# Kernel optimization log

Measured on AMD Instinct MI355X. Metric: run time of the kernel, lower is better.

Reference implementation:

```python
import jax, jax.numpy as jnp
import numpy as np

D = 1024        # model dim (== moe_inter_dim, required by Expert's x2*x3)
H = 1024        # expert hidden dim (moe_inter_dim)
E = 8           # n_routed_experts
K = 2           # n_activated_experts (top-k)
I = 2 * 1024    # shared-expert inter dim = n_shared_experts * moe_inter_dim
ROUTE_SCALE = 1.0


def setup_inputs() -> dict:
    key = jax.random.key(0)
    ks = jax.random.split(key, 12)
    s = lambda *sh: 1.0 / np.sqrt(sh[-1])
    return {
        "x":      jax.random.normal(ks[0], (1, 2048, D), jnp.float32),
        "gate_w": jax.random.normal(ks[1], (E, D), jnp.float32) * s(E, D),
        "w1":     jax.random.normal(ks[2], (E, H, D), jnp.float32) * s(H, D),
        "b1":     jax.random.normal(ks[3], (E, H), jnp.float32) * 0.01,
        "w2":     jax.random.normal(ks[4], (E, D, H), jnp.float32) * s(D, H),
        "b2":     jax.random.normal(ks[5], (E, D), jnp.float32) * 0.01,
        "w3":     jax.random.normal(ks[6], (E, H, D), jnp.float32) * s(H, D),
        "b3":     jax.random.normal(ks[7], (E, H), jnp.float32) * 0.01,
        "sw1":    jax.random.normal(ks[8], (I, D), jnp.float32) * s(I, D),
        "sw2":    jax.random.normal(ks[9], (I, D), jnp.float32) * s(I, D),
        "sw3":    jax.random.normal(ks[10], (D, I), jnp.float32) * s(D, I),
    }


def reference(x, gate_w, w1, b1, w2, b2, w3, b3, sw1, sw2, sw3):
    B, S, _ = x.shape
    xt = x.reshape(-1, D)                                  # (T, D)
    # ---- Gate (softmax scoring, n_groups==1, no bias, route_scale=1) ----
    logits = xt @ gate_w.T                                 # (T, E)
    scores = jax.nn.softmax(logits.astype(jnp.float32), axis=-1)
    top_vals, idx = jax.lax.top_k(scores, K)               # (T, K)
    weights = (jnp.take_along_axis(scores, idx, axis=1)
               .astype(x.dtype)) * ROUTE_SCALE             # (T, K)
    # ---- Routed experts: input is scaled by routing weight BEFORE expert ----
    xs = xt[:, None, :] * weights[:, :, None]              # (T, K, D)
    y = jnp.zeros_like(xt)
    for e in range(E):  # fixed small loop over experts (dense masked dispatch)
        mask = (idx == e).astype(x.dtype)                  # (T, K)
        h = jax.nn.silu(jnp.einsum('tkd,hd->tkh', xs, w1[e]) + b1[e])
        x2 = jnp.einsum('tkh,dh->tkd', h, w2[e]) + b2[e]   # (T, K, D)
        x3 = jnp.einsum('tkd,hd->tkh', xs, w3[e]) + b3[e]  # (T, K, H==D)
        y = y + jnp.sum((x2 * x3) * mask[:, :, None], axis=1)
    # ---- Shared experts (SwiGLU MLP, no biases) ----
    z = (jax.nn.silu(xt @ sw1.T) * (xt @ sw2.T)) @ sw3.T   # (T, D)
    return (y + z).reshape(B, S, D)
```

## Files before the change

kernel.cpp:

```cpp
#include <hip/hip_runtime.h>

typedef unsigned short u16;
typedef __attribute__((ext_vector_type(4))) float floatx4;
typedef __attribute__((ext_vector_type(8))) short short8;

#define MAXROWS 5120
#define MAXMT 40

__device__ __forceinline__ u16 f2bf(float f) {
    union { float f; unsigned u; } v; v.f = f;
    unsigned r = v.u + 0x7FFF + ((v.u >> 16) & 1);
    return (u16)(r >> 16);
}
__device__ __forceinline__ float bf2f(u16 h) {
    union { unsigned u; float f; } v; v.u = ((unsigned)h) << 16; return v.f;
}
__device__ __forceinline__ float silu_f(float x) { return x / (1.f + __expf(-x)); }

__device__ __forceinline__ void gl_lds16(const void* g, void* l) {
    __builtin_amdgcn_global_load_lds(
        (__attribute__((address_space(1))) unsigned int*)g,
        (__attribute__((address_space(3))) unsigned int*)l, 16, 0, 0);
}

__device__ __forceinline__ void ld_frags(
    unsigned a0, unsigned a1, unsigned a2, unsigned a3,
    unsigned b0, unsigned b1, unsigned b2, unsigned b3,
    short8& af0, short8& af1, short8& af2, short8& af3,
    short8& bf0, short8& bf1, short8& bf2, short8& bf3) {
    asm volatile(
        "ds_read_b128 %0, %8\n\t"
        "ds_read_b128 %1, %9\n\t"
        "ds_read_b128 %2, %10\n\t"
        "ds_read_b128 %3, %11\n\t"
        "ds_read_b128 %4, %12\n\t"
        "ds_read_b128 %5, %13\n\t"
        "ds_read_b128 %6, %14\n\t"
        "ds_read_b128 %7, %15\n\t"
        "s_waitcnt lgkmcnt(0)"
        : "=&v"(af0), "=&v"(af1), "=&v"(af2), "=&v"(af3),
          "=&v"(bf0), "=&v"(bf1), "=&v"(bf2), "=&v"(bf3)
        : "v"(a0), "v"(a1), "v"(a2), "v"(a3),
          "v"(b0), "v"(b1), "v"(b2), "v"(b3));
}

#define WAIT_VM4() __builtin_amdgcn_s_waitcnt(3956)
#define WAIT_VM0() __builtin_amdgcn_s_waitcnt(3952)
#define BAR()      __builtin_amdgcn_s_barrier()

__global__ void conv_gate(const float* __restrict__ w1, const float* __restrict__ w2,
                          const float* __restrict__ w3, const float* __restrict__ sw1,
                          const float* __restrict__ sw2, const float* __restrict__ sw3,
                          const float* __restrict__ x, const float* __restrict__ gw,
                          u16* __restrict__ W13, u16* __restrict__ W2b,
                          u16* __restrict__ S12, u16* __restrict__ S3b,
                          u16* __restrict__ Xb,
                          int* __restrict__ idxA, float* __restrict__ wA) {
    int bid = blockIdx.x;
    if (bid < 512) {
        int w = threadIdx.x >> 6, lane = threadIdx.x & 63;
        int t = bid * 4 + w;
        const float* xr = x + (size_t)t * 1024;
        float acc[8];
#pragma unroll
        for (int e = 0; e < 8; e++) acc[e] = 0.f;
#pragma unroll
        for (int i = 0; i < 16; i++) {
            float xv = xr[lane + (i << 6)];
#pragma unroll
            for (int e = 0; e < 8; e++) acc[e] += xv * gw[e * 1024 + lane + (i << 6)];
        }
#pragma unroll
        for (int e = 0; e < 8; e++)
            for (int off = 32; off > 0; off >>= 1) acc[e] += __shfl_xor(acc[e], off);
        if (lane == 0) {
            float m = acc[0];
#pragma unroll
            for (int e = 1; e < 8; e++) m = fmaxf(m, acc[e]);
            float p[8], s = 0.f;
#pragma unroll
            for (int e = 0; e < 8; e++) { p[e] = __expf(acc[e] - m); s += p[e]; }
            float inv = 1.f / s;
#pragma unroll
            for (int e = 0; e < 8; e++) p[e] *= inv;
            int i0 = 0;
#pragma unroll
            for (int e = 1; e < 8; e++) if (p[e] > p[i0]) i0 = e;
            int i1 = (i0 == 0) ? 1 : 0;
            for (int e = i1 + 1; e < 8; e++) if (e != i0 && p[e] > p[i1]) i1 = e;
            idxA[2 * t] = i0; idxA[2 * t + 1] = i1;
            wA[2 * t] = p[i0]; wA[2 * t + 1] = p[i1];
        }
        return;
    }
    long j = (long)(bid - 512) * 256 + threadIdx.x;
    const float* src; u16* dst; long d;
    if (j < 2097152) {
        long e = j >> 18; src = w1; dst = W13; d = j + (e << 18);
    } else if ((j -= 2097152) < 2097152) {
        long e = j >> 18; src = w3; dst = W13; d = j + (e << 18) + 262144;
    } else if ((j -= 2097152) < 2097152) { src = w2;  dst = W2b; d = j; }
    else if ((j -= 2097152) < 524288) {
        long rr = j >> 8, c4 = j & 255;
        long br = ((rr >> 4) << 5) + (rr & 15);
        src = sw1; dst = S12; d = (br << 8) + c4;
    } else if ((j -= 524288) < 524288) {
        long rr = j >> 8, c4 = j & 255;
        long br = ((rr >> 4) << 5) + 16 + (rr & 15);
        src = sw2; dst = S12; d = (br << 8) + c4;
    } else if ((j -= 524288) < 524288)     { src = sw3; dst = S3b; d = j; }
    else { j -= 524288; src = x; dst = Xb; d = j; }
    float4 v = ((const float4*)src)[j];
    ushort4 o; o.x = f2bf(v.x); o.y = f2bf(v.y); o.z = f2bf(v.z); o.w = f2bf(v.w);
    ((ushort4*)dst)[d] = o;
}

__global__ void rank_k(const int* __restrict__ idxA, int* __restrict__ tileexp,
                       int* __restrict__ ntiles, int* __restrict__ slot_of) {
    int lane = threadIdx.x;
    const int* my = idxA + lane * 64;
    int h[8];
#pragma unroll
    for (int e = 0; e < 8; e++) h[e] = 0;
    for (int i = 0; i < 64; i++) {
        int v = my[i];
#pragma unroll
        for (int e = 0; e < 8; e++) h[e] += (v == e);
    }
    int excl[8], tot[8];
#pragma unroll
    for (int e = 0; e < 8; e++) {
        int inc = h[e];
        for (int off = 1; off < 64; off <<= 1) {
            int up = __shfl_up(inc, off);
            if (lane >= off) inc += up;
        }
        excl[e] = inc - h[e];
        tot[e] = __shfl(inc, 63);
    }
    int base[8], tiles = 0;
#pragma unroll
    for (int e = 0; e < 8; e++) {
        base[e] = tiles * 128;
        tiles += (tot[e] + 127) >> 7;
    }
    if (lane == 0) {
        ntiles[0] = tiles;
        int t = 0;
        for (int e = 0; e < 8; e++) {
            int te = (tot[e] + 127) >> 7;
            for (int j = 0; j < te; j++) tileexp[t++] = e;
        }
    }
    int c[8];
#pragma unroll
    for (int e = 0; e < 8; e++) c[e] = base[e] + excl[e];
    for (int i = 0; i < 64; i++) {
        int v = my[i], slot = 0;
#pragma unroll
        for (int e = 0; e < 8; e++) slot += (v == e) ? c[e] : 0;
#pragma unroll
        for (int e = 0; e < 8; e++) c[e] += (v == e);
        slot_of[lane * 64 + i] = slot;
    }
}

__global__ void build_xs(const float* __restrict__ x, const float* __restrict__ wA,
                         const int* __restrict__ slot_of, u16* __restrict__ XS) {
    int s = blockIdx.x, i = threadIdx.x;
    int t = s >> 1; float w = wA[s]; int slot = slot_of[s];
    float4 v = ((const float4*)(x + (size_t)t * 1024))[i];
    ushort4 o; o.x = f2bf(v.x * w); o.y = f2bf(v.y * w); o.z = f2bf(v.z * w); o.w = f2bf(v.w * w);
    ((ushort4*)(XS + (size_t)slot * 1024))[i] = o;
}

#define STAGE32(BUF, Ab, Bb, lda, kk)                                          \
    {                                                                          \
        _Pragma("unroll")                                                      \
        for (int t = 0; t < 2; t++) {                                          \
            int r = (w << 4) + (t << 6) + rloc;                                \
            int cg = clds ^ ((r >> 1) & 3);                                    \
            gl_lds16(Ab + (size_t)(m0 + r) * (lda) + (kk) + (cg << 3),         \
                     LDS + (BUF)*4096 + ((w << 4) + (t << 6)) * 32);           \
            gl_lds16(Bb + (size_t)(n0 + r) * (lda) + (kk) + (cg << 3),         \
                     LDS + 8192 + (BUF)*4096 + ((w << 4) + (t << 6)) * 32);    \
        }                                                                      \
    }

#define COMPUTE32(BUF)                                                         \
    {                                                                          \
        short8 af[4], bf[4];                                                   \
        ld_frags(adA[0] + (BUF)*8192, adA[1] + (BUF)*8192,                     \
                 adA[2] + (BUF)*8192, adA[3] + (BUF)*8192,                     \
                 adB[0] + (BUF)*8192, adB[1] + (BUF)*8192,                     \
                 adB[2] + (BUF)*8192, adB[3] + (BUF)*8192,                     \
                 af[0], af[1], af[2], af[3], bf[0], bf[1], bf[2], bf[3]);      \
        _Pragma("unroll")                                                      \
        for (int i = 0; i < 4; i++)                                            \
            _Pragma("unroll")                                                  \
            for (int j = 0; j < 4; j++)                                        \
                acc[i][j] = __builtin_amdgcn_mfma_f32_16x16x32_bf16(           \
                    af[i], bf[j], acc[i][j], 0, 0, 0);                         \
    }

#define KLOOP(NP, Ab, Bb, lda, kbeg)                                           \
    {                                                                          \
        STAGE32(0, Ab, Bb, lda, (kbeg));                                       \
        for (int ii = 0; ii < (NP); ii++) {                                    \
            int kk = (kbeg) + (ii << 6);                                       \
            STAGE32(1, Ab, Bb, lda, kk + 32);                                  \
            WAIT_VM4(); BAR();                                                 \
            COMPUTE32(0);                                                      \
            BAR();                                                             \
            if (ii + 1 < (NP)) {                                               \
                STAGE32(0, Ab, Bb, lda, kk + 64);                              \
                WAIT_VM4();                                                    \
            } else {                                                           \
                WAIT_VM0();                                                    \
            }                                                                  \
            BAR();                                                             \
            COMPUTE32(1);                                                      \
            BAR();                                                             \
        }                                                                      \
    }

#define GEMM_PRE()                                                             \
    int tid = threadIdx.x, w = tid >> 6, lane = tid & 63;                      \
    int wm = w >> 1, wn = w & 1;                                               \
    int rloc = lane >> 2, clds = lane & 3, q = lane >> 4, l15 = lane & 15;     \
    unsigned ldsbase = (unsigned)(size_t)(__attribute__((address_space(3))) u16*)LDS; \
    unsigned adA[4], adB[4];                                                   \
    _Pragma("unroll")                                                          \
    for (int i = 0; i < 4; i++) {                                              \
        int rr = (wm << 6) + (i << 4) + l15;                                   \
        int g = q ^ ((rr >> 1) & 3);                                           \
        adA[i] = ldsbase + rr * 64 + g * 16;                                   \
    }                                                                          \
    _Pragma("unroll")                                                          \
    for (int j = 0; j < 4; j++) {                                              \
        int rr = (wn << 6) + (j << 4) + l15;                                   \
        int g = q ^ ((rr >> 1) & 3);                                           \
        adB[j] = ldsbase + 16384 + rr * 64 + g * 16;                           \
    }                                                                          \
    floatx4 acc[4][4];                                                         \
    _Pragma("unroll")                                                          \
    for (int i = 0; i < 4; i++)                                                \
        _Pragma("unroll")                                                      \
        for (int j = 0; j < 4; j++) {                                          \
            floatx4 z = {0.f, 0.f, 0.f, 0.f}; acc[i][j] = z;                   \
        }

__global__ __launch_bounds__(256) void gemm_A(
    const u16* __restrict__ XS, const u16* __restrict__ Xb,
    const u16* __restrict__ W13, const u16* __restrict__ S12,
    const float* __restrict__ b1, const float* __restrict__ b3,
    u16* __restrict__ H, u16* __restrict__ X3h, u16* __restrict__ G,
    const int* __restrict__ tileexp, const int* __restrict__ ntiles) {
    __shared__ u16 LDS[16384];
    int xcd = blockIdx.x & 7, ws = blockIdx.x >> 3;
    const u16 *Ab, *Bb; int mt, nt, e = 0; bool routed;
    if (ws < 80) {
        routed = true;
        mt = xcd * 5 + (ws >> 4);
        nt = ws & 15;
        if (mt >= ntiles[0]) return;
        e = tileexp[mt];
        Ab = XS; Bb = W13 + ((size_t)e << 21);
    } else {
        routed = false; int s = ws - 80;
        mt = ((xcd >> 2) << 3) + (s >> 3);
        nt = ((xcd & 3) << 3) + (s & 7);
        Ab = Xb; Bb = S12;
    }
    int m0 = mt * 128, n0 = nt * 128;
    GEMM_PRE();

    KLOOP(16, Ab, Bb, 1024, 0);

    if (routed) {
#pragma unroll
        for (int i = 0; i < 4; i++) {
            int rowb = m0 + (wm << 6) + (i << 4) + (q << 2);
#pragma unroll
            for (int j = 0; j < 4; j++) {
                int col = n0 + (wn << 6) + (j << 4) + l15;
#pragma unroll
                for (int r = 0; r < 4; r++) {
                    float v = acc[i][j][r];
                    int rw = rowb + r;
                    if (nt < 8) {
                        H[(size_t)rw * 1024 + col] = f2bf(silu_f(v + b1[e * 1024 + col]));
                    } else {
                        int c2 = col - 1024;
                        X3h[(size_t)rw * 1024 + c2] = f2bf(v + b3[e * 1024 + c2]);
                    }
                }
            }
        }
    } else {
#pragma unroll
        for (int i = 0; i < 4; i++) {
            int rowb = m0 + (wm << 6) + (i << 4) + (q << 2);
#pragma unroll
            for (int jp = 0; jp < 4; jp += 2) {
                int brb = n0 + (wn << 6) + (jp << 4);
                int lcol = ((brb >> 5) << 4) + l15;
#pragma unroll
                for (int r = 0; r < 4; r++) {
                    float u = acc[i][jp][r], v = acc[i][jp + 1][r];
                    G[(size_t)(rowb + r) * 2048 + lcol] = f2bf(silu_f(u) * v);
                }
            }
        }
    }
}

__global__ __launch_bounds__(256) void gemm_B(
    const u16* __restrict__ H, const u16* __restrict__ G,
    const u16* __restrict__ W2b, const u16* __restrict__ S3b,
    const float* __restrict__ b2, const u16* __restrict__ X3h,
    u16* __restrict__ P0, u16* __restrict__ P1,
    float* __restrict__ Z0, float* __restrict__ Z1,
    const int* __restrict__ tileexp, const int* __restrict__ ntiles) {
    __shared__ u16 LDS[16384];
    int xcd = blockIdx.x & 7, ws = blockIdx.x >> 3;
    const u16 *Ab, *Bb; int mt, nt, kc, lda, kbeg, np, e = 0; bool routed;
    if (ws < 80) {
        routed = true;
        mt = xcd * 5 + (ws >> 4);
        int r = ws & 15; nt = r & 7; kc = r >> 3;
        if (mt >= ntiles[0]) return;
        e = tileexp[mt];
        Ab = H; Bb = W2b + ((size_t)e << 20); lda = 1024; kbeg = kc << 9; np = 8;
    } else {
        routed = false; int s = ws - 80;
        kc = s & 1; int s2 = s >> 1;
        mt = ((xcd >> 1) << 2) + (s2 >> 2);
        nt = ((xcd & 1) << 2) + (s2 & 3);
        Ab = G; Bb = S3b; lda = 2048; kbeg = kc << 10; np = 16;
    }
    int m0 = mt * 128, n0 = nt * 128;
    GEMM_PRE();

    KLOOP(np, Ab, Bb, lda, kbeg);

    if (routed) {
        u16* Pk = kc ? P1 : P0;
#pragma unroll
        for (int i = 0; i < 4; i++) {
            int rowb = m0 + (wm << 6) + (i << 4) + (q << 2);
#pragma unroll
            for (int j = 0; j < 4; j++) {
                int col = n0 + (wn << 6) + (j << 4) + l15;
#pragma unroll
                for (int r = 0; r < 4; r++) {
                    int rw = rowb + r;
                    float v = acc[i][j][r] + (kc == 0 ? b2[e * 1024 + col] : 0.f);
                    float pv = v * bf2f(X3h[(size_t)rw * 1024 + col]);
                    Pk[(size_t)rw * 1024 + col] = f2bf(pv);
                }
            }
        }
    } else {
        float* Zk = kc ? Z1 : Z0;
#pragma unroll
        for (int i = 0; i < 4; i++) {
            int rowb = m0 + (wm << 6) + (i << 4) + (q << 2);
#pragma unroll
            for (int j = 0; j < 4; j++) {
                int col = n0 + (wn << 6) + (j << 4) + l15;
#pragma unroll
                for (int r = 0; r < 4; r++)
                    Zk[(size_t)(rowb + r) * 1024 + col] = acc[i][j][r];
            }
        }
    }
}

__global__ void final_k(const float* __restrict__ Z0, const float* __restrict__ Z1,
                        const u16* __restrict__ P0, const u16* __restrict__ P1,
                        const int* __restrict__ slot_of, float* __restrict__ out) {
    int i = blockIdx.x * 256 + threadIdx.x;
    int t = i >> 8, c4 = i & 255;
    int s0 = slot_of[2 * t], s1 = slot_of[2 * t + 1];
    float4 z0 = ((const float4*)Z0)[(size_t)t * 256 + c4];
    float4 z1 = ((const float4*)Z1)[(size_t)t * 256 + c4];
    ushort4 a0 = ((const ushort4*)P0)[(size_t)s0 * 256 + c4];
    ushort4 a1 = ((const ushort4*)P1)[(size_t)s0 * 256 + c4];
    ushort4 c0 = ((const ushort4*)P0)[(size_t)s1 * 256 + c4];
    ushort4 c1 = ((const ushort4*)P1)[(size_t)s1 * 256 + c4];
    float4 o;
    o.x = z0.x + z1.x + bf2f(a0.x) + bf2f(a1.x) + bf2f(c0.x) + bf2f(c1.x);
    o.y = z0.y + z1.y + bf2f(a0.y) + bf2f(a1.y) + bf2f(c0.y) + bf2f(c1.y);
    o.z = z0.z + z1.z + bf2f(a0.z) + bf2f(a1.z) + bf2f(c0.z) + bf2f(c1.z);
    o.w = z0.w + z1.w + bf2f(a0.w) + bf2f(a1.w) + bf2f(c0.w) + bf2f(c1.w);
    ((float4*)out)[(size_t)t * 256 + c4] = o;
}

extern "C" void kernel_launch(void* const* d_in, const int* in_sizes, int n_in,
                              void* d_out, int out_size, void* d_ws, size_t ws_size,
                              hipStream_t stream) {
    const float* x   = (const float*)d_in[0];
    const float* gw  = (const float*)d_in[1];
    const float* w1  = (const float*)d_in[2];
    const float* b1  = (const float*)d_in[3];
    const float* w2  = (const float*)d_in[4];
    const float* b2  = (const float*)d_in[5];
    const float* w3  = (const float*)d_in[6];
    const float* b3  = (const float*)d_in[7];
    const float* sw1 = (const float*)d_in[8];
    const float* sw2 = (const float*)d_in[9];
    const float* sw3 = (const float*)d_in[10];
    float* out = (float*)d_out;

    char* p = (char*)d_ws;
    int* ntiles  = (int*)(p + 192);
    int* tileexp = (int*)(p + 256);
    size_t off = 4096;
    u16*   XS      = (u16*)(p + off);   off += (size_t)MAXROWS * 1024 * 2;
    int*   idxA    = (int*)(p + off);   off += 16384;
    float* wA      = (float*)(p + off); off += 16384;
    int*   slot_of = (int*)(p + off);   off += 16384;
    u16*   H       = (u16*)(p + off);   off += (size_t)MAXROWS * 1024 * 2;
    u16*   X3h     = (u16*)(p + off);   off += (size_t)MAXROWS * 1024 * 2;
    u16*   P0      = (u16*)(p + off);   off += (size_t)MAXROWS * 1024 * 2;
    u16*   P1      = (u16*)(p + off);   off += (size_t)MAXROWS * 1024 * 2;
    float* Z0      = (float*)(p + off); off += (size_t)2048 * 1024 * 4;
    float* Z1      = (float*)(p + off); off += (size_t)2048 * 1024 * 4;
    u16*   W13     = (u16*)(p + off);   off += (size_t)8 * 2048 * 1024 * 2;
    u16*   W2b     = (u16*)(p + off);   off += (size_t)8 * 1024 * 1024 * 2;
    u16*   S12     = (u16*)(p + off);   off += (size_t)4096 * 1024 * 2;
    u16*   S3b     = (u16*)(p + off);   off += (size_t)1024 * 2048 * 2;
    u16*   Xb      = (u16*)(p + off);   off += (size_t)2048 * 1024 * 2;
    u16*   G       = (u16*)(p + off);   off += (size_t)2048 * 2048 * 2;

    conv_gate<<<33280, 256, 0, stream>>>(w1, w2, w3, sw1, sw2, sw3, x, gw,
                                         W13, W2b, S12, S3b, Xb, idxA, wA);
    rank_k<<<1, 64, 0, stream>>>(idxA, tileexp, ntiles, slot_of);
    build_xs<<<4096, 256, 0, stream>>>(x, wA, slot_of, XS);

    gemm_A<<<1152, 256, 0, stream>>>(XS, Xb, W13, S12, b1, b3, H, X3h, G,
                                     tileexp, ntiles);
    gemm_B<<<896, 256, 0, stream>>>(H, G, W2b, S3b, b2, X3h, P0, P1, Z0, Z1,
                                    tileexp, ntiles);
    final_k<<<2048, 256, 0, stream>>>(Z0, Z1, P0, P1, slot_of, out);
}
```

Before: 310.7 us.

## Switch GEMMs to 128x256 tiles with 512 threads and single-buffered LDS

Both grouped GEMM kernels move from 128x128 tiles with 256 threads and a hand-written double-buffered k-loop (inline asm ds_reads, vmcnt waits) to 128x256 tiles with 512 threads (2x4 waves). Each stage now loads a 64-wide K slice with an XOR-8 swizzle and uses plain __syncthreads around a compiler-generated compute. The larger N tile increases reuse of the A operand and halves the block count. In exchange it gives up the explicit overlap of global loads with MFMA, so load latency may be exposed, and fewer blocks reduce the number of tiles available to spread across CUs.

```diff
diff --git a/kernel.cpp b/kernel.cpp
--- a/kernel.cpp
+++ b/kernel.cpp
@@ -22,31 +22,6 @@
         (__attribute__((address_space(1))) unsigned int*)g,
         (__attribute__((address_space(3))) unsigned int*)l, 16, 0, 0);
 }
-
-__device__ __forceinline__ void ld_frags(
-    unsigned a0, unsigned a1, unsigned a2, unsigned a3,
-    unsigned b0, unsigned b1, unsigned b2, unsigned b3,
-    short8& af0, short8& af1, short8& af2, short8& af3,
-    short8& bf0, short8& bf1, short8& bf2, short8& bf3) {
-    asm volatile(
-        "ds_read_b128 %0, %8\n\t"
-        "ds_read_b128 %1, %9\n\t"
-        "ds_read_b128 %2, %10\n\t"
-        "ds_read_b128 %3, %11\n\t"
-        "ds_read_b128 %4, %12\n\t"
-        "ds_read_b128 %5, %13\n\t"
-        "ds_read_b128 %6, %14\n\t"
-        "ds_read_b128 %7, %15\n\t"
-        "s_waitcnt lgkmcnt(0)"
-        : "=&v"(af0), "=&v"(af1), "=&v"(af2), "=&v"(af3),
-          "=&v"(bf0), "=&v"(bf1), "=&v"(bf2), "=&v"(bf3)
-        : "v"(a0), "v"(a1), "v"(a2), "v"(a3),
-          "v"(b0), "v"(b1), "v"(b2), "v"(b3));
-}
-
-#define WAIT_VM4() __builtin_amdgcn_s_waitcnt(3956)
-#define WAIT_VM0() __builtin_amdgcn_s_waitcnt(3952)
-#define BAR()      __builtin_amdgcn_s_barrier()
 
 __global__ void conv_gate(const float* __restrict__ w1, const float* __restrict__ w2,
                           const float* __restrict__ w3, const float* __restrict__ sw1,
@@ -174,74 +149,54 @@
     ((ushort4*)(XS + (size_t)slot * 1024))[i] = o;
 }
 
-#define STAGE32(BUF, Ab, Bb, lda, kk)                                          \
+#define STAGE(Ab, Bb, lda, kk)                                                 \
     {                                                                          \
         _Pragma("unroll")                                                      \
         for (int t = 0; t < 2; t++) {                                          \
-            int r = (w << 4) + (t << 6) + rloc;                                \
-            int cg = clds ^ ((r >> 1) & 3);                                    \
+            int r = (w << 4) + (t << 3) + rloc;                                \
+            int cg = clds ^ (r & 7);                                           \
             gl_lds16(Ab + (size_t)(m0 + r) * (lda) + (kk) + (cg << 3),         \
-                     LDS + (BUF)*4096 + ((w << 4) + (t << 6)) * 32);           \
+                     &LDS[((w << 4) + (t << 3)) << 6]);                        \
+        }                                                                      \
+        _Pragma("unroll")                                                      \
+        for (int t = 0; t < 4; t++) {                                          \
+            int r = (w << 5) + (t << 3) + rloc;                                \
+            int cg = clds ^ (r & 7);                                           \
             gl_lds16(Bb + (size_t)(n0 + r) * (lda) + (kk) + (cg << 3),         \
-                     LDS + 8192 + (BUF)*4096 + ((w << 4) + (t << 6)) * 32);    \
+                     &LDS[8192 + (((w << 5) + (t << 3)) << 6)]);               \
         }                                                                      \
     }
 
-#define COMPUTE32(BUF)                                                         \
+#define COMPUTE()                                                              \
     {                                                                          \
-        short8 af[4], bf[4];                                                   \
-        ld_frags(adA[0] + (BUF)*8192, adA[1] + (BUF)*8192,                     \
-                 adA[2] + (BUF)*8192, adA[3] + (BUF)*8192,                     \
-                 adB[0] + (BUF)*8192, adB[1] + (BUF)*8192,                     \
-                 adB[2] + (BUF)*8192, adB[3] + (BUF)*8192,                     \
-                 af[0], af[1], af[2], af[3], bf[0], bf[1], bf[2], bf[3]);      \
         _Pragma("unroll")                                                      \
-        for (int i = 0; i < 4; i++)                                            \
+        for (int hh = 0; hh < 2; hh++) {                                       \
+            short8 af[4], bf[4];                                               \
             _Pragma("unroll")                                                  \
-            for (int j = 0; j < 4; j++)                                        \
-                acc[i][j] = __builtin_amdgcn_mfma_f32_16x16x32_bf16(           \
-                    af[i], bf[j], acc[i][j], 0, 0, 0);                         \
-    }
-
-#define KLOOP(NP, Ab, Bb, lda, kbeg)                                           \
-    {                                                                          \
-        STAGE32(0, Ab, Bb, lda, (kbeg));                                       \
-        for (int ii = 0; ii < (NP); ii++) {                                    \
-            int kk = (kbeg) + (ii << 6);                                       \
-            STAGE32(1, Ab, Bb, lda, kk + 32);                                  \
-            WAIT_VM4(); BAR();                                                 \
-            COMPUTE32(0);                                                      \
-            BAR();                                                             \
-            if (ii + 1 < (NP)) {                                               \
-                STAGE32(0, Ab, Bb, lda, kk + 64);                              \
-                WAIT_VM4();                                                    \
-            } else {                                                           \
-                WAIT_VM0();                                                    \
+            for (int i = 0; i < 4; i++) {                                      \
+                int rr = (wm << 6) + (i << 4) + l15;                           \
+                int sl = ((hh << 2) + q) ^ (rr & 7);                           \
+                af[i] = *(const short8*)&LDS[(rr << 6) + (sl << 3)];           \
             }                                                                  \
-            BAR();                                                             \
-            COMPUTE32(1);                                                      \
-            BAR();                                                             \
+            _Pragma("unroll")                                                  \
+            for (int j = 0; j < 4; j++) {                                      \
+                int rr = (wn << 6) + (j << 4) + l15;                           \
+                int sl = ((hh << 2) + q) ^ (rr & 7);                           \
+                bf[j] = *(const short8*)&LDS[8192 + (rr << 6) + (sl << 3)];    \
+            }                                                                  \
+            _Pragma("unroll")                                                  \
+            for (int i = 0; i < 4; i++)                                        \
+                _Pragma("unroll")                                              \
+                for (int j = 0; j < 4; j++)                                    \
+                    acc[i][j] = __builtin_amdgcn_mfma_f32_16x16x32_bf16(       \
+                        af[i], bf[j], acc[i][j], 0, 0, 0);                     \
         }                                                                      \
     }
 
 #define GEMM_PRE()                                                             \
     int tid = threadIdx.x, w = tid >> 6, lane = tid & 63;                      \
-    int wm = w >> 1, wn = w & 1;                                               \
-    int rloc = lane >> 2, clds = lane & 3, q = lane >> 4, l15 = lane & 15;     \
-    unsigned ldsbase = (unsigned)(size_t)(__attribute__((address_space(3))) u16*)LDS; \
-    unsigned adA[4], adB[4];                                                   \
-    _Pragma("unroll")                                                          \
-    for (int i = 0; i < 4; i++) {                                              \
-        int rr = (wm << 6) + (i << 4) + l15;                                   \
-        int g = q ^ ((rr >> 1) & 3);                                           \
-        adA[i] = ldsbase + rr * 64 + g * 16;                                   \
-    }                                                                          \
-    _Pragma("unroll")                                                          \
-    for (int j = 0; j < 4; j++) {                                              \
-        int rr = (wn << 6) + (j << 4) + l15;                                   \
-        int g = q ^ ((rr >> 1) & 3);                                           \
-        adB[j] = ldsbase + 16384 + rr * 64 + g * 16;                           \
-    }                                                                          \
+    int wm = w >> 2, wn = w & 3;                                               \
+    int rloc = lane >> 3, clds = lane & 7, q = lane >> 4, l15 = lane & 15;     \
     floatx4 acc[4][4];                                                         \
     _Pragma("unroll")                                                          \
     for (int i = 0; i < 4; i++)                                                \
@@ -250,32 +205,37 @@
             floatx4 z = {0.f, 0.f, 0.f, 0.f}; acc[i][j] = z;                   \
         }
 
-__global__ __launch_bounds__(256) void gemm_A(
+__global__ __launch_bounds__(512, 4) void gemm_A(
     const u16* __restrict__ XS, const u16* __restrict__ Xb,
     const u16* __restrict__ W13, const u16* __restrict__ S12,
     const float* __restrict__ b1, const float* __restrict__ b3,
     u16* __restrict__ H, u16* __restrict__ X3h, u16* __restrict__ G,
     const int* __restrict__ tileexp, const int* __restrict__ ntiles) {
-    __shared__ u16 LDS[16384];
+    __shared__ u16 LDS[24576];
     int xcd = blockIdx.x & 7, ws = blockIdx.x >> 3;
     const u16 *Ab, *Bb; int mt, nt, e = 0; bool routed;
-    if (ws < 80) {
+    if (ws < 40) {
         routed = true;
-        mt = xcd * 5 + (ws >> 4);
-        nt = ws & 15;
+        mt = xcd * 5 + (ws >> 3);
+        nt = ws & 7;
         if (mt >= ntiles[0]) return;
         e = tileexp[mt];
         Ab = XS; Bb = W13 + ((size_t)e << 21);
     } else {
-        routed = false; int s = ws - 80;
-        mt = ((xcd >> 2) << 3) + (s >> 3);
-        nt = ((xcd & 3) << 3) + (s & 7);
+        routed = false; int s = ws - 40;
+        mt = xcd * 2 + (s >> 4);
+        nt = s & 15;
         Ab = Xb; Bb = S12;
     }
-    int m0 = mt * 128, n0 = nt * 128;
+    int m0 = mt * 128, n0 = nt * 256;
     GEMM_PRE();
 
-    KLOOP(16, Ab, Bb, 1024, 0);
+    for (int k0 = 0; k0 < 1024; k0 += 64) {
+        STAGE(Ab, Bb, 1024, k0);
+        __syncthreads();
+        COMPUTE();
+        __syncthreads();
+    }
 
     if (routed) {
 #pragma unroll
@@ -288,7 +248,7 @@
                 for (int r = 0; r < 4; r++) {
                     float v = acc[i][j][r];
                     int rw = rowb + r;
-                    if (nt < 8) {
+                    if (nt < 4) {
                         H[(size_t)rw * 1024 + col] = f2bf(silu_f(v + b1[e * 1024 + col]));
                     } else {
                         int c2 = col - 1024;
@@ -315,34 +275,38 @@
     }
 }
 
-__global__ __launch_bounds__(256) void gemm_B(
+__global__ __launch_bounds__(512, 4) void gemm_B(
     const u16* __restrict__ H, const u16* __restrict__ G,
     const u16* __restrict__ W2b, const u16* __restrict__ S3b,
     const float* __restrict__ b2, const u16* __restrict__ X3h,
     u16* __restrict__ P0, u16* __restrict__ P1,
     float* __restrict__ Z0, float* __restrict__ Z1,
     const int* __restrict__ tileexp, const int* __restrict__ ntiles) {
-    __shared__ u16 LDS[16384];
+    __shared__ u16 LDS[24576];
     int xcd = blockIdx.x & 7, ws = blockIdx.x >> 3;
-    const u16 *Ab, *Bb; int mt, nt, kc, lda, kbeg, np, e = 0; bool routed;
-    if (ws < 80) {
+    const u16 *Ab, *Bb; int mt, nt, kc, lda, kbeg, kend, e = 0; bool routed;
+    if (ws < 40) {
         routed = true;
-        mt = xcd * 5 + (ws >> 4);
-        int r = ws & 15; nt = r & 7; kc = r >> 3;
+        mt = xcd * 5 + (ws >> 3);
+        int r = ws & 7; nt = r & 3; kc = r >> 2;
         if (mt >= ntiles[0]) return;
         e = tileexp[mt];
-        Ab = H; Bb = W2b + ((size_t)e << 20); lda = 1024; kbeg = kc << 9; np = 8;
+        Ab = H; Bb = W2b + ((size_t)e << 20); lda = 1024; kbeg = kc << 9; kend = kbeg + 512;
     } else {
-        routed = false; int s = ws - 80;
-        kc = s & 1; int s2 = s >> 1;
-        mt = ((xcd >> 1) << 2) + (s2 >> 2);
-        nt = ((xcd & 1) << 2) + (s2 & 3);
-        Ab = G; Bb = S3b; lda = 2048; kbeg = kc << 10; np = 16;
-    }
-    int m0 = mt * 128, n0 = nt * 128;
+        routed = false; int s = ws - 40;
+        mt = xcd * 2 + (s >> 3);
+        int r = s & 7; nt = r & 3; kc = r >> 2;
+        Ab = G; Bb = S3b; lda = 2048; kbeg = kc << 10; kend = kbeg + 1024;
+    }
+    int m0 = mt * 128, n0 = nt * 256;
     GEMM_PRE();
 
-    KLOOP(np, Ab, Bb, lda, kbeg);
+    for (int k0 = kbeg; k0 < kend; k0 += 64) {
+        STAGE(Ab, Bb, lda, k0);
+        __syncthreads();
+        COMPUTE();
+        __syncthreads();
+    }
 
     if (routed) {
         u16* Pk = kc ? P1 : P0;
@@ -439,9 +403,9 @@
     rank_k<<<1, 64, 0, stream>>>(idxA, tileexp, ntiles, slot_of);
     build_xs<<<4096, 256, 0, stream>>>(x, wA, slot_of, XS);
 
-    gemm_A<<<1152, 256, 0, stream>>>(XS, Xb, W13, S12, b1, b3, H, X3h, G,
-                                     tileexp, ntiles);
-    gemm_B<<<896, 256, 0, stream>>>(H, G, W2b, S3b, b2, X3h, P0, P1, Z0, Z1,
+    gemm_A<<<576, 512, 0, stream>>>(XS, Xb, W13, S12, b1, b3, H, X3h, G,
+                                    tileexp, ntiles);
+    gemm_B<<<448, 512, 0, stream>>>(H, G, W2b, S3b, b2, X3h, P0, P1, Z0, Z1,
                                     tileexp, ntiles);
     final_k<<<2048, 256, 0, stream>>>(Z0, Z1, P0, P1, slot_of, out);
 }
```

After: 321.5 us. 3.5% more time.
